# Kernel tuning notes

Hardware: AMD Instinct MI355X
Metric: run time of the kernel (lower is better)

Reference implementation:

```python
import jax, jax.numpy as jnp
import numpy as np

B, D, L, H = 2048, 64, 64, 512  # batch, in_dim, latent_space, hidden


def setup_inputs() -> dict:
    key = jax.random.key(0)
    ks = jax.random.split(key, 12)
    inp = {
        "x": jax.random.normal(ks[0], (B, D), jnp.float32),
        "koopman": jax.random.normal(ks[1], (B, L, D), jnp.float32),
    }
    dims = [(L, H), (H, H), (H, H), (H, D)]
    k = 2
    for pfx in ("s", "t"):
        for j, (fi, fo) in enumerate(dims):
            inp[f"{pfx}W{j+1}"] = jax.random.normal(ks[k], (fi, fo), jnp.float32) / np.sqrt(fi).astype(np.float32)
            inp[f"{pfx}b{j+1}"] = jnp.zeros((fo,), jnp.float32)
            k += 1
    return inp


def _mlp(z, W1, b1, W2, b2, W3, b3, W4, b4):
    h = jnp.tanh(z @ W1 + b1)
    h = jnp.tanh(h @ W2 + b2)
    h = jnp.tanh(h @ W3 + b3)
    return h @ W4 + b4


def reference(x, koopman,
              sW1, sb1, sW2, sb2, sW3, sb3, sW4, sb4,
              tW1, tb1, tW2, tb2, tW3, tb3, tW4, tb4):
    # koopman: (B, L, D) -> z: (B, D, L); column i of the torch loop is z[:, i, :]
    z = jnp.swapaxes(koopman, 1, 2)
    s = _mlp(z, sW1, sb1, sW2, sb2, sW3, sb3, sW4, sb4)  # (B, D, D)
    t = _mlp(z, tW1, tb1, tW2, tb2, tW3, tb3, tW4, tb4)  # (B, D, D)
    # loop kept only output column i for input column i -> diagonal over last two dims
    ds = jnp.diagonal(s, axis1=1, axis2=2)  # (B, D)
    dt = jnp.diagonal(t, axis1=1, axis2=2)  # (B, D)
    return (x - dt) * jnp.exp(-ds)
```

## Files before the change

kernel.cpp:

```cpp
#include <hip/hip_runtime.h>


typedef _Float16 f16;
typedef _Float16 f16x8 __attribute__((ext_vector_type(8)));
typedef float f32x16 __attribute__((ext_vector_type(16)));

#define WPACK_PER_NET 589824
#define OFF_W1 0
#define OFF_W2 32768
#define OFF_W3 294912
#define OFF_W4T 557056
#define WPACK_BYTES (2u * WPACK_PER_NET * sizeof(f16))

__device__ __forceinline__ void lds_barrier() {
  asm volatile("s_waitcnt lgkmcnt(0)\n\ts_barrier" ::: "memory");
}

__global__ void pack_weights(const float* __restrict__ sW1, const float* __restrict__ sW2,
                             const float* __restrict__ sW3, const float* __restrict__ sW4,
                             const float* __restrict__ tW1, const float* __restrict__ tW2,
                             const float* __restrict__ tW3, const float* __restrict__ tW4,
                             f16* __restrict__ dst) {
  int idx = blockIdx.x * 256 + threadIdx.x;
  int net = idx >= WPACK_PER_NET;
  int f = idx - net * WPACK_PER_NET;
  const float* W;
  int base;
  if (f < OFF_W2) {
    W = net ? tW1 : sW1; base = OFF_W1;
  } else if (f < OFF_W3) {
    W = net ? tW2 : sW2; base = OFF_W2;
  } else if (f < OFF_W4T) {
    W = net ? tW3 : sW3; base = OFF_W3;
  } else {
    int f4 = f - OFF_W4T;
    dst[idx] = (f16)((net ? tW4 : sW4)[(f4 & 511) * 64 + (f4 >> 9)]);
    return;
  }
  int fl = f - base;
  int j = fl & 7, ln = (fl >> 3) & 63, nt = (fl >> 9) & 1, w = (fl >> 10) & 7,
      s = fl >> 13;
  dst[idx] = (f16)W[(s * 16 + (ln >> 5) * 8 + j) * 512 + w * 64 + nt * 32 + (ln & 31)];
}

__device__ __forceinline__ int aidx2(int m, int k) {
  return (((k >> 4) * 4 + (m >> 5)) * 64 + (m & 31) + ((k >> 3) & 1) * 32) * 8 + (k & 7);
}

__device__ __forceinline__ int swz(int idx) {
  return idx ^ (((idx >> 8) & 1) << 3) ^ (((idx >> 11) & 1) << 4);
}

__device__ __forceinline__ float fast_tanh(float x) {
  float e = __expf(x + x);
  return fmaf(-2.0f, __builtin_amdgcn_rcpf(e + 1.0f), 1.0f);
}

template <int NS2>
__device__ __forceinline__ void mlp_layer(const char* __restrict__ wlb,
                                          const float* __restrict__ bias,
                                          const f16* Asrc, f16* Hout,
                                          int wave, int lane, int sbase,
                                          int sx, int rl0, int rl1) {
  f32x16 acc[4][2];
  {
    float bv0 = bias[wave * 64 + (lane & 31)];
    float bv1 = bias[wave * 64 + 32 + (lane & 31)];
#pragma unroll
    for (int mt = 0; mt < 4; mt++)
#pragma unroll
      for (int r = 0; r < 16; r++) {
        acc[mt][0][r] = bv0;
        acc[mt][1][r] = bv1;
      }
  }
  f16x8 bb[2][2], aa[2][4];
  bb[0][0] = *(const f16x8*)(wlb);
  bb[0][1] = *(const f16x8*)(wlb + 1024);
  {
    const f16* a0 = Asrc + rl0;
#pragma unroll
    for (int mt = 0; mt < 4; mt++) aa[0][mt] = *(const f16x8*)(a0 + mt * 512);
  }
#pragma unroll
  for (int s = 0; s < NS2; s++) {
    if (s + 1 < NS2) {
      const char* q = wlb + (s + 1) * 16384;
      bb[(s + 1) & 1][0] = *(const f16x8*)(q);
      bb[(s + 1) & 1][1] = *(const f16x8*)(q + 1024);
      const f16* an = Asrc + (s + 1) * 2048 + (((s + 1) & 1) ? rl1 : rl0);
#pragma unroll
      for (int mt = 0; mt < 4; mt++)
        aa[(s + 1) & 1][mt] = *(const f16x8*)(an + mt * 512);
    }
#pragma unroll
    for (int mt = 0; mt < 4; mt++) {
      acc[mt][0] = __builtin_amdgcn_mfma_f32_32x32x16_f16(aa[s & 1][mt], bb[s & 1][0],
                                                          acc[mt][0], 0, 0, 0);
      acc[mt][1] = __builtin_amdgcn_mfma_f32_32x32x16_f16(aa[s & 1][mt], bb[s & 1][1],
                                                          acc[mt][1], 0, 0, 0);
    }
  }
  lds_barrier();
  f16* hx[4];
#pragma unroll
  for (int v = 0; v < 4; v++) hx[v] = Hout + sbase + ((v ^ sx) << 3);
#pragma unroll
  for (int mt = 0; mt < 4; mt++)
#pragma unroll
    for (int nt = 0; nt < 2; nt++)
#pragma unroll
      for (int r = 0; r < 16; r++)
        hx[r & 3][nt * 4096 + mt * 512 + (r >> 2) * 64] =
            (f16)fast_tanh(acc[mt][nt][r]);
  lds_barrier();
}

__global__ __launch_bounds__(512, 2) void decoder_main(
    const float* __restrict__ x, const float* __restrict__ koop,
    const f16* __restrict__ wpack,
    const float* __restrict__ sb1, const float* __restrict__ sb2,
    const float* __restrict__ sb3, const float* __restrict__ sb4,
    const float* __restrict__ tb1, const float* __restrict__ tb2,
    const float* __restrict__ tb3, const float* __restrict__ tb4,
    float* __restrict__ out) {
  __shared__ __align__(16) f16 ZA[8192];
  __shared__ __align__(16) f16 HA[65536];
  __shared__ float redBuf[2][128];

  const int b = blockIdx.x;
  const int t = threadIdx.x;
  const int wave = t >> 6, lane = t & 63;
  const int ln5 = lane & 31, q5 = lane >> 5;
  const int sx = (lane >> 3) & 3;
  const int rl0 = (lane ^ q5) * 8;
  const int rl1 = rl0 ^ 16;
  const int sbase = wave * 8192 + (ln5 >> 4) * 2048 + ((ln5 >> 3) & 1) * 256 +
                    q5 * 32 + (ln5 & 7);
  const char* wbb = (const char*)wpack + wave * 2048 + lane * 16;

  const float* kb = koop + (size_t)b * 8192;
#pragma unroll
  for (int i = 0; i < 16; i++) {
    int flat = t + 512 * i;
    int bi = flat >> 12, rem = flat & 4095;
    ZA[swz(aidx2(bi * 64 + (rem & 63), rem >> 6))] = (f16)kb[flat];
  }
  lds_barrier();

  for (int net = 0; net < 2; net++) {
    const size_t nb = (size_t)net * (WPACK_PER_NET * 2);
    const float* b1 = net ? tb1 : sb1;
    const float* b2 = net ? tb2 : sb2;
    const float* b3 = net ? tb3 : sb3;
    const float* b4 = net ? tb4 : sb4;
    mlp_layer<4>(wbb + nb + OFF_W1 * 2, b1, ZA, HA, wave, lane, sbase, sx, rl0, rl1);
    mlp_layer<32>(wbb + nb + OFF_W2 * 2, b2, HA, HA, wave, lane, sbase, sx, rl0, rl1);
    mlp_layer<32>(wbb + nb + OFF_W3 * 2, b3, HA, HA, wave, lane, sbase, sx, rl0, rl1);

    const f16* w4t = wpack + net * WPACK_PER_NET + OFF_W4T;
    int i2 = t >> 2, sub = t & 3;
    float p = 0.f;
#pragma unroll
    for (int qq = 0; qq < 16; qq++) {
      int k0 = sub * 128 + qq * 8;
      f16x8 hv = *(const f16x8*)&HA[swz(aidx2(i2, k0))];
      f16x8 wv = *(const f16x8*)&w4t[(i2 & 63) * 512 + k0];
#pragma unroll
      for (int j = 0; j < 8; j++) p += (float)hv[j] * (float)wv[j];
    }
    p += __shfl_down(p, 2, 4);
    p += __shfl_down(p, 1, 4);
    if (sub == 0) redBuf[net][i2] = p + b4[i2 & 63];
    lds_barrier();
  }

  if (t < 128) {
    out[b * 128 + t] = (x[b * 128 + t] - redBuf[1][t]) * __expf(-redBuf[0][t]);
  }
}

typedef float f32x4 __attribute__((ext_vector_type(4)));

__device__ __forceinline__ int aidx(int m, int k) {
  return (((k >> 5) * 4 + (m >> 4)) * 64 + (m & 15) + ((k >> 3) & 3) * 16) * 8 + (k & 7);
}

__device__ __forceinline__ void load_b_direct(const float* __restrict__ Wraw,
                                              int kk, int wave, int lane,
                                              f16x8* bdst) {
  int n0 = wave * 64 + (lane & 15);
  int kb = kk * 32 + (lane >> 4) * 8;
#pragma unroll
  for (int nt = 0; nt < 4; nt++) {
    f16x8 v;
#pragma unroll
    for (int j = 0; j < 8; j++) v[j] = (f16)Wraw[(kb + j) * 512 + n0 + nt * 16];
    bdst[nt] = v;
  }
}

template <int NS>
__device__ __forceinline__ void mlp_layer_direct(
    const float* __restrict__ Wraw, const float* __restrict__ bias,
    const f16* Asrc, f16* Hout, int wave, int lane, int sbase) {
  f32x4 acc[4][4];
#pragma unroll
  for (int nt = 0; nt < 4; nt++) {
    float bv = bias[wave * 64 + nt * 16 + (lane & 15)];
#pragma unroll
    for (int mt = 0; mt < 4; mt++) acc[mt][nt] = f32x4{bv, bv, bv, bv};
  }
  f16x8 bb[2][4];
  load_b_direct(Wraw, 0, wave, lane, bb[0]);
#pragma unroll
  for (int kk = 0; kk < NS; kk++) {
    if (kk + 1 < NS) load_b_direct(Wraw, kk + 1, wave, lane, bb[(kk + 1) & 1]);
    const f16* ab = Asrc + kk * 2048 + lane * 8;
#pragma unroll
    for (int mt = 0; mt < 4; mt++) {
      f16x8 a = *(const f16x8*)(ab + mt * 512);
#pragma unroll
      for (int nt = 0; nt < 4; nt++)
        acc[mt][nt] = __builtin_amdgcn_mfma_f32_16x16x32_f16(a, bb[kk & 1][nt],
                                                             acc[mt][nt], 0, 0, 0);
    }
  }
  __syncthreads();
  f16* hb = Hout + sbase;
#pragma unroll
  for (int mt = 0; mt < 4; mt++)
#pragma unroll
    for (int nt = 0; nt < 4; nt++)
#pragma unroll
      for (int r = 0; r < 4; r++)
        hb[(nt >> 1) * 2048 + mt * 512 + (nt & 1) * 256 + r * 8] =
            (f16)fast_tanh(acc[mt][nt][r]);
  __syncthreads();
}

__global__ __launch_bounds__(512, 4) void decoder_direct(
    const float* __restrict__ x, const float* __restrict__ koop,
    const float* __restrict__ sW1, const float* __restrict__ sW2,
    const float* __restrict__ sW3, const float* __restrict__ sW4,
    const float* __restrict__ tW1, const float* __restrict__ tW2,
    const float* __restrict__ tW3, const float* __restrict__ tW4,
    const float* __restrict__ sb1, const float* __restrict__ sb2,
    const float* __restrict__ sb3, const float* __restrict__ sb4,
    const float* __restrict__ tb1, const float* __restrict__ tb2,
    const float* __restrict__ tb3, const float* __restrict__ tb4,
    float* __restrict__ out) {
  __shared__ __align__(16) f16 ZA[4096];
  __shared__ __align__(16) f16 HA[32768];
  __shared__ float redBuf[2][64];
  const int b = blockIdx.x;
  const int t = threadIdx.x;
  const int wave = t >> 6, lane = t & 63;
  const int sbase =
      wave * 4096 + (lane >> 4) * 32 + ((lane & 15) >> 3) * 128 + (lane & 7);
  const float* kb = koop + b * 4096;
#pragma unroll
  for (int i = 0; i < 8; i++) {
    int flat = t + 512 * i;
    ZA[aidx(flat & 63, flat >> 6)] = (f16)kb[flat];
  }
  __syncthreads();
  for (int net = 0; net < 2; net++) {
    const float* W1 = net ? tW1 : sW1;
    const float* W2 = net ? tW2 : sW2;
    const float* W3 = net ? tW3 : sW3;
    const float* W4 = net ? tW4 : sW4;
    const float* b1 = net ? tb1 : sb1;
    const float* b2 = net ? tb2 : sb2;
    const float* b3 = net ? tb3 : sb3;
    const float* b4 = net ? tb4 : sb4;
    mlp_layer_direct<2>(W1, b1, ZA, HA, wave, lane, sbase);
    mlp_layer_direct<16>(W2, b2, HA, HA, wave, lane, sbase);
    mlp_layer_direct<16>(W3, b3, HA, HA, wave, lane, sbase);
    int i = t >> 3, sub = t & 7;
    float p = 0.f;
#pragma unroll
    for (int qq = 0; qq < 8; qq++) {
      int k0 = sub * 64 + qq * 8;
      f16x8 hv = *(const f16x8*)&HA[aidx(i, k0)];
#pragma unroll
      for (int j = 0; j < 8; j++) p += (float)hv[j] * W4[(k0 + j) * 64 + i];
    }
    p += __shfl_down(p, 4, 8);
    p += __shfl_down(p, 2, 8);
    p += __shfl_down(p, 1, 8);
    if (sub == 0) redBuf[net][i] = p + b4[i];
    __syncthreads();
  }
  if (t < 64) {
    out[b * 64 + t] = (x[b * 64 + t] - redBuf[1][t]) * __expf(-redBuf[0][t]);
  }
}

extern "C" void kernel_launch(void* const* d_in, const int* in_sizes, int n_in,
                              void* d_out, int out_size, void* d_ws, size_t ws_size,
                              hipStream_t stream) {
  const float* x    = (const float*)d_in[0];
  const float* koop = (const float*)d_in[1];
  const float* sW1 = (const float*)d_in[2];  const float* sb1 = (const float*)d_in[3];
  const float* sW2 = (const float*)d_in[4];  const float* sb2 = (const float*)d_in[5];
  const float* sW3 = (const float*)d_in[6];  const float* sb3 = (const float*)d_in[7];
  const float* sW4 = (const float*)d_in[8];  const float* sb4 = (const float*)d_in[9];
  const float* tW1 = (const float*)d_in[10]; const float* tb1 = (const float*)d_in[11];
  const float* tW2 = (const float*)d_in[12]; const float* tb2 = (const float*)d_in[13];
  const float* tW3 = (const float*)d_in[14]; const float* tb3 = (const float*)d_in[15];
  const float* tW4 = (const float*)d_in[16]; const float* tb4 = (const float*)d_in[17];
  float* out = (float*)d_out;

  if (ws_size >= (size_t)WPACK_BYTES) {
    f16* wpack = (f16*)d_ws;
    pack_weights<<<4608, 256, 0, stream>>>(sW1, sW2, sW3, sW4, tW1, tW2, tW3, tW4,
                                           wpack);
    decoder_main<<<1024, 512, 0, stream>>>(x, koop, wpack,
                                           sb1, sb2, sb3, sb4,
                                           tb1, tb2, tb3, tb4, out);
  } else {
    decoder_direct<<<2048, 512, 0, stream>>>(
        x, koop, sW1, sW2, sW3, sW4, tW1, tW2, tW3, tW4,
        sb1, sb2, sb3, sb4, tb1, tb2, tb3, tb4, out);
  }
}
```

Before: 444.7 us.

## Double waves per block, halving each wave's output column tile

Each block now runs 16 waves of 1024 threads instead of 8 waves of 512. Each wave computes a 128x32 output tile with one accumulator set instead of 128x64. The weight packing layout, LDS write offsets, koopman staging and final-layer dot-product split are all rewritten to match. A-operand prefetch double-buffering is dropped in favour of loading A fragments inline. The goal is more waves per CU to hide latency and lower register pressure, at the cost of each wave reading A from LDS twice as often per MFMA and more barrier participants.

Result: slower. 479.6 us (+7.8%).

```diff
diff --git a/kernel.cpp b/kernel.cpp
--- a/kernel.cpp
+++ b/kernel.cpp
@@ -38,9 +38,8 @@
     return;
   }
   int fl = f - base;
-  int j = fl & 7, ln = (fl >> 3) & 63, nt = (fl >> 9) & 1, w = (fl >> 10) & 7,
-      s = fl >> 13;
-  dst[idx] = (f16)W[(s * 16 + (ln >> 5) * 8 + j) * 512 + w * 64 + nt * 32 + (ln & 31)];
+  int j = fl & 7, ln = (fl >> 3) & 63, w = (fl >> 9) & 15, s = fl >> 13;
+  dst[idx] = (f16)W[(s * 16 + (ln >> 5) * 8 + j) * 512 + w * 32 + (ln & 31)];
 }
 
 __device__ __forceinline__ int aidx2(int m, int k) {
@@ -62,43 +61,24 @@
                                           const f16* Asrc, f16* Hout,
                                           int wave, int lane, int sbase,
                                           int sx, int rl0, int rl1) {
-  f32x16 acc[4][2];
+  f32x16 acc[4];
   {
-    float bv0 = bias[wave * 64 + (lane & 31)];
-    float bv1 = bias[wave * 64 + 32 + (lane & 31)];
+    float bv = bias[wave * 32 + (lane & 31)];
 #pragma unroll
     for (int mt = 0; mt < 4; mt++)
 #pragma unroll
-      for (int r = 0; r < 16; r++) {
-        acc[mt][0][r] = bv0;
-        acc[mt][1][r] = bv1;
-      }
-  }
-  f16x8 bb[2][2], aa[2][4];
-  bb[0][0] = *(const f16x8*)(wlb);
-  bb[0][1] = *(const f16x8*)(wlb + 1024);
-  {
-    const f16* a0 = Asrc + rl0;
-#pragma unroll
-    for (int mt = 0; mt < 4; mt++) aa[0][mt] = *(const f16x8*)(a0 + mt * 512);
-  }
+      for (int r = 0; r < 16; r++) acc[mt][r] = bv;
+  }
+  f16x8 bb[2];
+  bb[0] = *(const f16x8*)(wlb);
 #pragma unroll
   for (int s = 0; s < NS2; s++) {
-    if (s + 1 < NS2) {
-      const char* q = wlb + (s + 1) * 16384;
-      bb[(s + 1) & 1][0] = *(const f16x8*)(q);
-      bb[(s + 1) & 1][1] = *(const f16x8*)(q + 1024);
-      const f16* an = Asrc + (s + 1) * 2048 + (((s + 1) & 1) ? rl1 : rl0);
-#pragma unroll
-      for (int mt = 0; mt < 4; mt++)
-        aa[(s + 1) & 1][mt] = *(const f16x8*)(an + mt * 512);
-    }
+    if (s + 1 < NS2) bb[(s + 1) & 1] = *(const f16x8*)(wlb + (s + 1) * 16384);
+    const f16* ab = Asrc + s * 2048 + ((s & 1) ? rl1 : rl0);
 #pragma unroll
     for (int mt = 0; mt < 4; mt++) {
-      acc[mt][0] = __builtin_amdgcn_mfma_f32_32x32x16_f16(aa[s & 1][mt], bb[s & 1][0],
-                                                          acc[mt][0], 0, 0, 0);
-      acc[mt][1] = __builtin_amdgcn_mfma_f32_32x32x16_f16(aa[s & 1][mt], bb[s & 1][1],
-                                                          acc[mt][1], 0, 0, 0);
+      f16x8 a = *(const f16x8*)(ab + mt * 512);
+      acc[mt] = __builtin_amdgcn_mfma_f32_32x32x16_f16(a, bb[s & 1], acc[mt], 0, 0, 0);
     }
   }
   lds_barrier();
@@ -108,15 +88,12 @@
 #pragma unroll
   for (int mt = 0; mt < 4; mt++)
 #pragma unroll
-    for (int nt = 0; nt < 2; nt++)
-#pragma unroll
-      for (int r = 0; r < 16; r++)
-        hx[r & 3][nt * 4096 + mt * 512 + (r >> 2) * 64] =
-            (f16)fast_tanh(acc[mt][nt][r]);
+    for (int r = 0; r < 16; r++)
+      hx[r & 3][mt * 512 + (r >> 2) * 64] = (f16)fast_tanh(acc[mt][r]);
   lds_barrier();
 }
 
-__global__ __launch_bounds__(512, 2) void decoder_main(
+__global__ __launch_bounds__(1024, 4) void decoder_main(
     const float* __restrict__ x, const float* __restrict__ koop,
     const f16* __restrict__ wpack,
     const float* __restrict__ sb1, const float* __restrict__ sb2,
@@ -135,14 +112,14 @@
   const int sx = (lane >> 3) & 3;
   const int rl0 = (lane ^ q5) * 8;
   const int rl1 = rl0 ^ 16;
-  const int sbase = wave * 8192 + (ln5 >> 4) * 2048 + ((ln5 >> 3) & 1) * 256 +
+  const int sbase = wave * 4096 + (ln5 >> 4) * 2048 + ((ln5 >> 3) & 1) * 256 +
                     q5 * 32 + (ln5 & 7);
-  const char* wbb = (const char*)wpack + wave * 2048 + lane * 16;
+  const char* wbb = (const char*)wpack + wave * 1024 + lane * 16;
 
   const float* kb = koop + (size_t)b * 8192;
 #pragma unroll
-  for (int i = 0; i < 16; i++) {
-    int flat = t + 512 * i;
+  for (int i = 0; i < 8; i++) {
+    int flat = t + 1024 * i;
     int bi = flat >> 12, rem = flat & 4095;
     ZA[swz(aidx2(bi * 64 + (rem & 63), rem >> 6))] = (f16)kb[flat];
   }
@@ -159,18 +136,19 @@
     mlp_layer<32>(wbb + nb + OFF_W3 * 2, b3, HA, HA, wave, lane, sbase, sx, rl0, rl1);
 
     const f16* w4t = wpack + net * WPACK_PER_NET + OFF_W4T;
-    int i2 = t >> 2, sub = t & 3;
+    int i2 = t >> 3, sub = t & 7;
     float p = 0.f;
 #pragma unroll
-    for (int qq = 0; qq < 16; qq++) {
-      int k0 = sub * 128 + qq * 8;
+    for (int qq = 0; qq < 8; qq++) {
+      int k0 = sub * 64 + qq * 8;
       f16x8 hv = *(const f16x8*)&HA[swz(aidx2(i2, k0))];
       f16x8 wv = *(const f16x8*)&w4t[(i2 & 63) * 512 + k0];
 #pragma unroll
       for (int j = 0; j < 8; j++) p += (float)hv[j] * (float)wv[j];
     }
-    p += __shfl_down(p, 2, 4);
-    p += __shfl_down(p, 1, 4);
+    p += __shfl_down(p, 4, 8);
+    p += __shfl_down(p, 2, 8);
+    p += __shfl_down(p, 1, 8);
     if (sub == 0) redBuf[net][i2] = p + b4[i2 & 63];
     lds_barrier();
   }
@@ -316,9 +294,9 @@
     f16* wpack = (f16*)d_ws;
     pack_weights<<<4608, 256, 0, stream>>>(sW1, sW2, sW3, sW4, tW1, tW2, tW3, tW4,
                                            wpack);
-    decoder_main<<<1024, 512, 0, stream>>>(x, koop, wpack,
-                                           sb1, sb2, sb3, sb4,
-                                           tb1, tb2, tb3, tb4, out);
+    decoder_main<<<1024, 1024, 0, stream>>>(x, koop, wpack,
+                                            sb1, sb2, sb3, sb4,
+                                            tb1, tb2, tb3, tb4, out);
   } else {
     decoder_direct<<<2048, 512, 0, stream>>>(
         x, koop, sW1, sW2, sW3, sW4, tW1, tW2, tW3, tW4,
```
